# Optimization experiments

Measured on AMD Instinct MI355X. Metric: run time of the kernel, lower is better.

Reference implementation:

```python
import jax, jax.numpy as jnp
import numpy as np

QDIM = 1024; KDIM = 2048; NH = 16; HD = QDIM // NH
H = 64; W = 64; B = 8; S2 = 256
EPS = 1e-6; SCALE = HD ** -0.5


def setup_inputs() -> dict:
    key = jax.random.key(0)
    ks = jax.random.split(key, 8)
    def lin(k, fan_in, shape):
        lim = 1.0 / np.sqrt(fan_in)
        return jax.random.uniform(k, shape, jnp.float32, -lim, lim)
    return {
        "x": jax.random.normal(ks[0], (B, H * W, QDIM), jnp.float32),
        "y": jax.random.normal(ks[1], (B, S2, KDIM), jnp.float32),
        "wq": lin(ks[2], QDIM, (QDIM, QDIM)),
        "bq": lin(ks[3], QDIM, (QDIM,)),
        "wkv": lin(ks[4], KDIM, (2 * QDIM, KDIM)),
        "bkv": lin(ks[5], KDIM, (2 * QDIM,)),
        "wo": lin(ks[6], QDIM, (QDIM, QDIM)),
        "bo": lin(ks[7], QDIM, (QDIM,)),
        "qn_g": jnp.ones((HD,), jnp.float32),
        "qn_b": jnp.zeros((HD,), jnp.float32),
        "kn_g": jnp.ones((HD,), jnp.float32),
        "kn_b": jnp.zeros((HD,), jnp.float32),
    }


def _layernorm(t, g, b):
    mu = t.mean(-1, keepdims=True)
    var = ((t - mu) ** 2).mean(-1, keepdims=True)
    return (t - mu) * jax.lax.rsqrt(var + EPS) * g + b


def _rope_2d_angles():
    # Lumina-style 2D rotary: head_dim//2 complex freqs per position,
    # interleaving H-axis and W-axis frequencies along the pair dim.
    d4 = HD // 4
    inv = 1.0 / (10000.0 ** (np.arange(0, HD // 2, 2, dtype=np.float32) / (HD // 2)))  # (d4,)
    fh = np.outer(np.arange(H, dtype=np.float32), inv)  # (H, d4)
    fw = np.outer(np.arange(W, dtype=np.float32), inv)  # (W, d4)
    ang = np.stack([
        np.broadcast_to(fh[:, None, :], (H, W, d4)),
        np.broadcast_to(fw[None, :, :], (H, W, d4)),
    ], axis=-1).reshape(H, W, HD // 2)  # interleaved h,w,h,w,...
    return jnp.asarray(np.cos(ang)), jnp.asarray(np.sin(ang))


def reference(x, y, wq, bq, wkv, bkv, wo, bo, qn_g, qn_b, kn_g, kn_b):
    b, s1, c = x.shape
    q = (x @ wq.T + bq).reshape(b, s1, NH, HD).transpose(0, 2, 1, 3)          # (b, nh, s1, hd)
    kv = (y @ wkv.T + bkv).reshape(b, -1, 2, NH, HD).transpose(0, 2, 3, 1, 4)  # (b, 2, nh, s2, hd)
    k, v = kv[:, 0], kv[:, 1]
    q = _layernorm(q, qn_g, qn_b)
    k = _layernorm(k, kn_g, kn_b)
    # inline 2D RoPE on Q only (complex mult on interleaved pairs)
    cos, sin = _rope_2d_angles()                                               # (H, W, hd//2)
    qr = q.reshape(b, NH, H, W, HD // 2, 2)
    qe, qo = qr[..., 0], qr[..., 1]
    q = jnp.stack([qe * cos - qo * sin, qe * sin + qo * cos], axis=-1).reshape(b, NH, s1, HD)
    attn = jax.nn.softmax((q * SCALE) @ jnp.swapaxes(k, -2, -1), axis=-1)      # (b, nh, s1, s2)
    out = (attn @ v).transpose(0, 2, 1, 3).reshape(b, s1, c)
    return out @ wo.T + bo
```

## Files before the change

kernel.cpp:

```cpp
#include <hip/hip_runtime.h>
#include <hip/hip_bf16.h>

typedef __bf16 bf16x8 __attribute__((ext_vector_type(8)));
typedef __bf16 bf16x4 __attribute__((ext_vector_type(4)));
typedef float f32x4 __attribute__((ext_vector_type(4)));

__device__ __forceinline__ void async_copy16(__bf16* lds_base, const __bf16* g) {
  __builtin_amdgcn_global_load_lds(
      (const __attribute__((address_space(1))) void*)g,
      (__attribute__((address_space(3))) void*)lds_base, 16, 0, 0);
}

__global__ __launch_bounds__(256) void cvt_bf16(const float* __restrict__ in,
                                                __bf16* __restrict__ out, int n4) {
  int i = blockIdx.x * 256 + threadIdx.x;
  if (i >= n4) return;
  float4 v = ((const float4*)in)[i];
  bf16x4 o;
  o.x = (__bf16)v.x; o.y = (__bf16)v.y; o.z = (__bf16)v.z; o.w = (__bf16)v.w;
  ((bf16x4*)out)[i] = o;
}

template<bool STORE_BF16>
__global__ __launch_bounds__(256) void gemm_bt(const __bf16* __restrict__ A,
                                               const __bf16* __restrict__ Bw,
                                               const float* __restrict__ bias,
                                               void* __restrict__ Cp,
                                               int M, int N, int K) {
  __shared__ __align__(16) __bf16 sA[128 * 64];
  __shared__ __align__(16) __bf16 sB[128 * 64];
  const int tid = threadIdx.x;
  const int lane = tid & 63;
  const int w = tid >> 6;
  const int wr = w >> 1, wc = w & 1;
  const int l15 = lane & 15, q4 = lane >> 4;
  const int bm = blockIdx.x, bn = blockIdx.y;

  f32x4 acc[4][4] = {};

  for (int k0 = 0; k0 < K; k0 += 64) {
    __syncthreads();
#pragma unroll
    for (int it = 0; it < 4; ++it) {
      int chunk = it * 256 + tid;
      int row = chunk >> 3, c8 = chunk & 7;
      int ldsbase = (it * 256 + w * 64) * 8;
      async_copy16(sA + ldsbase, A + (size_t)(bm * 128 + row) * K + k0 + c8 * 8);
      async_copy16(sB + ldsbase, Bw + (size_t)(bn * 128 + row) * K + k0 + c8 * 8);
    }
    __syncthreads();
#pragma unroll
    for (int kk = 0; kk < 2; ++kk) {
      bf16x8 af[4], bfr[4];
#pragma unroll
      for (int i = 0; i < 4; ++i)
        af[i] = *(const bf16x8*)(sA + (wr * 64 + i * 16 + l15) * 64 + kk * 32 + q4 * 8);
#pragma unroll
      for (int j = 0; j < 4; ++j)
        bfr[j] = *(const bf16x8*)(sB + (wc * 64 + j * 16 + l15) * 64 + kk * 32 + q4 * 8);
#pragma unroll
      for (int i = 0; i < 4; ++i)
#pragma unroll
        for (int j = 0; j < 4; ++j)
          acc[i][j] = __builtin_amdgcn_mfma_f32_16x16x32_bf16(af[i], bfr[j], acc[i][j], 0, 0, 0);
    }
  }
#pragma unroll
  for (int j = 0; j < 4; ++j) {
    const int col = bn * 128 + wc * 64 + j * 16 + l15;
    const float bv = bias[col];
#pragma unroll
    for (int i = 0; i < 4; ++i) {
      const int row0 = bm * 128 + wr * 64 + i * 16 + q4 * 4;
#pragma unroll
      for (int r = 0; r < 4; ++r) {
        float v = acc[i][j][r] + bv;
        size_t off = (size_t)(row0 + r) * N + col;
        if (STORE_BF16) ((__bf16*)Cp)[off] = (__bf16)v;
        else            ((float*)Cp)[off]  = v;
      }
    }
  }
}

template<int KK, bool STORE_BF16>
__global__ __launch_bounds__(512, 2) void gemm_bt_big(const __bf16* __restrict__ A,
                                                      const __bf16* __restrict__ Bw,
                                                      const float* __restrict__ bias,
                                                      void* __restrict__ Cp,
                                                      int N) {
  static_assert(KK % 32 == 0 && KK / 32 >= 4, "KK");
  constexpr int NT = KK / 32;
  __shared__ __align__(16) __bf16 sA[4 * 256 * 32];
  __shared__ __align__(16) __bf16 sB[4 * 256 * 32];
  const int tid = threadIdx.x;
  const int lane = tid & 63;
  const int w = tid >> 6;
  const int wr = w >> 2, wc = w & 3;
  const int l15 = lane & 15, q4 = lane >> 4;
  const int bm = blockIdx.x, bn = blockIdx.y;

  const int r0 = tid >> 2;
  const int csw = (tid & 3) ^ (r0 & 3);
  const __bf16* gA0 = A + (size_t)(bm * 256 + r0) * KK + csw * 8;
  const __bf16* gA1 = gA0 + (size_t)128 * KK;
  const __bf16* gB0 = Bw + (size_t)(bn * 256 + r0) * KK + csw * 8;
  const __bf16* gB1 = gB0 + (size_t)128 * KK;
  const int lds_w0 = (w * 64) * 8;
  const int lds_w1 = (512 + w * 64) * 8;

  const int qsw = (q4 ^ (l15 & 3)) * 8;
  const int aBase = (wr * 128 + l15) * 32 + qsw;
  const int bBase = (wc * 64 + l15) * 32 + qsw;

  f32x4 acc[8][4] = {};

#pragma unroll
  for (int t = 0; t < 3; ++t) {
    async_copy16(sA + t * 8192 + lds_w0, gA0 + t * 32);
    async_copy16(sA + t * 8192 + lds_w1, gA1 + t * 32);
    async_copy16(sB + t * 8192 + lds_w0, gB0 + t * 32);
    async_copy16(sB + t * 8192 + lds_w1, gB1 + t * 32);
  }
  asm volatile("s_waitcnt vmcnt(8)" ::: "memory");
  __builtin_amdgcn_s_barrier();
  __builtin_amdgcn_sched_barrier(0);

#pragma unroll 4
  for (int t = 0; t < NT; ++t) {
    const __bf16* sAs = sA + (t & 3) * 8192;
    const __bf16* sBs = sB + (t & 3) * 8192;
    const int ps = (t + 3) & 3;
    const bool pf = (t + 3) < NT;

    bf16x8 af[4], bfrag[4];
#pragma unroll
    for (int m = 0; m < 4; ++m)
      af[m] = *(const bf16x8*)(sAs + aBase + m * 512);
#pragma unroll
    for (int n = 0; n < 4; ++n)
      bfrag[n] = *(const bf16x8*)(sBs + bBase + n * 512);
    if (pf) {
      async_copy16(sA + ps * 8192 + lds_w0, gA0 + (t + 3) * 32);
      async_copy16(sA + ps * 8192 + lds_w1, gA1 + (t + 3) * 32);
    }
    __builtin_amdgcn_s_barrier();
    asm volatile("s_waitcnt lgkmcnt(0)" ::: "memory");
    __builtin_amdgcn_sched_barrier(0);
    __builtin_amdgcn_s_setprio(1);
#pragma unroll
    for (int m = 0; m < 4; ++m)
#pragma unroll
      for (int n = 0; n < 4; ++n)
        acc[m][n] = __builtin_amdgcn_mfma_f32_16x16x32_bf16(af[m], bfrag[n], acc[m][n], 0, 0, 0);
    __builtin_amdgcn_s_setprio(0);
    __builtin_amdgcn_s_barrier();
    __builtin_amdgcn_sched_barrier(0);

    bf16x8 ag[4];
#pragma unroll
    for (int m = 0; m < 4; ++m)
      ag[m] = *(const bf16x8*)(sAs + aBase + 2048 + m * 512);
    if (pf) {
      async_copy16(sB + ps * 8192 + lds_w0, gB0 + (t + 3) * 32);
      async_copy16(sB + ps * 8192 + lds_w1, gB1 + (t + 3) * 32);
    }
    if (pf)                 asm volatile("s_waitcnt vmcnt(8)" ::: "memory");
    else if (t + 3 == NT)   asm volatile("s_waitcnt vmcnt(4)" ::: "memory");
    else if (t + 2 == NT)   asm volatile("s_waitcnt vmcnt(0)" ::: "memory");
    __builtin_amdgcn_s_barrier();
    asm volatile("s_waitcnt lgkmcnt(0)" ::: "memory");
    __builtin_amdgcn_sched_barrier(0);
    __builtin_amdgcn_s_setprio(1);
#pragma unroll
    for (int m = 0; m < 4; ++m)
#pragma unroll
      for (int n = 0; n < 4; ++n)
        acc[4 + m][n] = __builtin_amdgcn_mfma_f32_16x16x32_bf16(ag[m], bfrag[n], acc[4 + m][n], 0, 0, 0);
    __builtin_amdgcn_s_setprio(0);
    __builtin_amdgcn_s_barrier();
    __builtin_amdgcn_sched_barrier(0);
  }

#pragma unroll
  for (int n = 0; n < 4; ++n) {
    const int col = bn * 256 + wc * 64 + n * 16 + l15;
    const float bv = bias[col];
#pragma unroll
    for (int m = 0; m < 8; ++m) {
      const int row0 = bm * 256 + wr * 128 + m * 16 + q4 * 4;
#pragma unroll
      for (int r = 0; r < 4; ++r) {
        float v = acc[m][n][r] + bv;
        size_t off = (size_t)(row0 + r) * N + col;
        if (STORE_BF16) ((__bf16*)Cp)[off] = (__bf16)v;
        else            ((float*)Cp)[off]  = v;
      }
    }
  }
}

__global__ __launch_bounds__(256) void kv_epilogue(const float* __restrict__ kv,
                                                   const float* __restrict__ g,
                                                   const float* __restrict__ bta,
                                                   __bf16* __restrict__ Kd,
                                                   __bf16* __restrict__ VT) {
  const int lane = threadIdx.x & 63;
  const int vec = blockIdx.x * 4 + (threadIdx.x >> 6);
  const int nh = vec & 15;
  const int sv = (vec >> 4) & 1;
  const int row = vec >> 5;
  const int b = row >> 8, s2 = row & 255;
  float v = kv[(size_t)row * 2048 + sv * 1024 + nh * 64 + lane];
  if (sv == 0) {
    float mu = v;
#pragma unroll
    for (int o = 32; o; o >>= 1) mu += __shfl_xor(mu, o);
    mu *= (1.f / 64.f);
    float d = v - mu;
    float va = d * d;
#pragma unroll
    for (int o = 32; o; o >>= 1) va += __shfl_xor(va, o);
    va *= (1.f / 64.f);
    float xn = d * rsqrtf(va + 1e-6f) * g[lane] + bta[lane];
    Kd[(((size_t)b * 16 + nh) * 256 + s2) * 64 + lane] = (__bf16)xn;
  } else {
    VT[(((size_t)b * 16 + nh) * 64 + lane) * 256 + s2] = (__bf16)v;
  }
}

__global__ __launch_bounds__(256) void q_epilogue(const __bf16* __restrict__ qraw,
                                                  const float* __restrict__ g,
                                                  const float* __restrict__ bta,
                                                  __bf16* __restrict__ Q) {
  const int lane = threadIdx.x & 63;
  const int vec = blockIdx.x * 4 + (threadIdx.x >> 6);
  const int nh = vec & 15;
  const int row = vec >> 4;
  float v = (float)qraw[(size_t)row * 1024 + nh * 64 + lane];
  float mu = v;
#pragma unroll
  for (int o = 32; o; o >>= 1) mu += __shfl_xor(mu, o);
  mu *= (1.f / 64.f);
  float d = v - mu;
  float va = d * d;
#pragma unroll
  for (int o = 32; o; o >>= 1) va += __shfl_xor(va, o);
  va *= (1.f / 64.f);
  float xn = d * rsqrtf(va + 1e-6f) * g[lane] + bta[lane];
  const int s1 = row & 4095;
  const int hh = s1 >> 6, wpix = s1 & 63;
  const int t = lane >> 2;
  const int usew = (lane >> 1) & 1;
  float inv = __expf(-(float)t * 0.5756462732485114f);
  float ang = (usew ? (float)wpix : (float)hh) * inv;
  float cc = __cosf(ang), ssn = __sinf(ang);
  float partner = __shfl_xor(xn, 1);
  float rot = xn * cc + partner * ssn * ((lane & 1) ? 1.f : -1.f);
  rot *= 0.125f;
  const int b = row >> 12;
  Q[(((size_t)b * 16 + nh) * 4096 + (size_t)s1) * 64 + lane] = (__bf16)rot;
}

__global__ __launch_bounds__(256) void attn_kernel(const __bf16* __restrict__ Q,
                                                   const __bf16* __restrict__ Kd,
                                                   const __bf16* __restrict__ VT,
                                                   __bf16* __restrict__ O) {
  __shared__ __align__(16) __bf16 sK[256 * 64];
  __shared__ __align__(16) __bf16 sV[64 * 256];
  const int tid = threadIdx.x, lane = tid & 63, w = tid >> 6;
  const int l15 = lane & 15, q4 = lane >> 4;
  const int s7 = l15 & 7;
  const int bh = blockIdx.y;
  const int m0 = blockIdx.x * 64;
  const __bf16* Kg = Kd + (size_t)bh * 256 * 64;
  const __bf16* Vg = VT + (size_t)bh * 64 * 256;
  const __bf16* Qg = Q + ((size_t)bh * 4096 + m0) * 64;
#pragma unroll
  for (int it = 0; it < 8; ++it) {
    int c = it * 256 + tid;
    int kr = c >> 3, kh = c & 7;
    *(uint4*)(sK + kr * 64 + ((kh ^ (kr & 7)) * 8)) = *(const uint4*)(Kg + c * 8);
    int vr = c >> 5, vh = c & 31;
    *(uint4*)(sV + vr * 256 + ((vh ^ (vr & 7)) * 8)) = *(const uint4*)(Vg + c * 8);
  }
  bf16x8 qf0 = *(const bf16x8*)(Qg + (w * 16 + l15) * 64 + q4 * 8);
  bf16x8 qf1 = *(const bf16x8*)(Qg + (w * 16 + l15) * 64 + 32 + q4 * 8);
  __syncthreads();
  f32x4 sacc[16] = {};
#pragma unroll
  for (int mt = 0; mt < 16; ++mt) {
    bf16x8 a0 = *(const bf16x8*)(sK + (mt * 16 + l15) * 64 + ((q4 ^ s7) * 8));
    bf16x8 a1 = *(const bf16x8*)(sK + (mt * 16 + l15) * 64 + (((4 + q4) ^ s7) * 8));
    sacc[mt] = __builtin_amdgcn_mfma_f32_16x16x32_bf16(a0, qf0, sacc[mt], 0, 0, 0);
    sacc[mt] = __builtin_amdgcn_mfma_f32_16x16x32_bf16(a1, qf1, sacc[mt], 0, 0, 0);
  }
  __syncthreads();
  float mx = -1e30f;
#pragma unroll
  for (int mt = 0; mt < 16; ++mt)
#pragma unroll
    for (int r = 0; r < 4; ++r) mx = fmaxf(mx, sacc[mt][r]);
  mx = fmaxf(mx, __shfl_xor(mx, 16));
  mx = fmaxf(mx, __shfl_xor(mx, 32));
  float l = 0.f;
#pragma unroll
  for (int mt = 0; mt < 16; ++mt)
#pragma unroll
    for (int r = 0; r < 4; ++r) {
      float p = __expf(sacc[mt][r] - mx);
      sacc[mt][r] = p;
      l += p;
    }
  l += __shfl_xor(l, 16);
  l += __shfl_xor(l, 32);
  const float linv = 1.f / l;
#pragma unroll
  for (int mt = 0; mt < 16; ++mt) {
    bf16x4 pk;
    pk.x = (__bf16)(sacc[mt][0] * linv);
    pk.y = (__bf16)(sacc[mt][1] * linv);
    pk.z = (__bf16)(sacc[mt][2] * linv);
    pk.w = (__bf16)(sacc[mt][3] * linv);
    int chunk = mt * 2 + (q4 >> 1);
    *(bf16x4*)(sK + (w * 16 + l15) * 256 + ((chunk ^ s7) * 8) + (q4 & 1) * 4) = pk;
  }
  f32x4 oacc[4] = {};
#pragma unroll
  for (int ks = 0; ks < 8; ++ks) {
    int phys = ((ks * 4 + q4) ^ s7) * 8;
    bf16x8 a = *(const bf16x8*)(sK + (w * 16 + l15) * 256 + phys);
#pragma unroll
    for (int j = 0; j < 4; ++j) {
      bf16x8 b = *(const bf16x8*)(sV + (j * 16 + l15) * 256 + phys);
      oacc[j] = __builtin_amdgcn_mfma_f32_16x16x32_bf16(a, b, oacc[j], 0, 0, 0);
    }
  }
  const int b = bh >> 4, nh = bh & 15;
#pragma unroll
  for (int j = 0; j < 4; ++j)
#pragma unroll
    for (int r = 0; r < 4; ++r) {
      size_t off = ((size_t)b * 4096 + m0 + w * 16 + q4 * 4 + r) * 1024
                 + nh * 64 + j * 16 + l15;
      O[off] = (__bf16)oacc[j][r];
    }
}

extern "C" void kernel_launch(void* const* d_in, const int* in_sizes, int n_in,
                              void* d_out, int out_size, void* d_ws, size_t ws_size,
                              hipStream_t stream) {
  const float* x    = (const float*)d_in[0];
  const float* y    = (const float*)d_in[1];
  const float* wq   = (const float*)d_in[2];
  const float* bq   = (const float*)d_in[3];
  const float* wkv  = (const float*)d_in[4];
  const float* bkv  = (const float*)d_in[5];
  const float* wo   = (const float*)d_in[6];
  const float* bo   = (const float*)d_in[7];
  const float* qng  = (const float*)d_in[8];
  const float* qnb  = (const float*)d_in[9];
  const float* kng  = (const float*)d_in[10];
  const float* knb  = (const float*)d_in[11];
  float* out = (float*)d_out;

  char* ws = (char*)d_ws;
  size_t off = 0;
  auto take = [&](size_t bytes) { char* p = ws + off; off += (bytes + 255) & ~(size_t)255; return p; };
  __bf16* xb   = (__bf16*)take((size_t)32768 * 1024 * 2);
  char*  reg1  = take((size_t)32768 * 1024 * 2);
  __bf16* Qb   = (__bf16*)take((size_t)32768 * 1024 * 2);
  __bf16* yb   = (__bf16*)take((size_t)2048 * 2048 * 2);
  __bf16* wqb  = (__bf16*)take((size_t)1024 * 1024 * 2);
  __bf16* wkvb = (__bf16*)take((size_t)2048 * 2048 * 2);
  __bf16* wob  = (__bf16*)take((size_t)1024 * 1024 * 2);
  __bf16* Kb   = (__bf16*)take((size_t)128 * 256 * 64 * 2);
  __bf16* VTb  = (__bf16*)take((size_t)128 * 64 * 256 * 2);
  float*  kvf  = (float*)reg1;
  __bf16* qraw = (__bf16*)reg1;
  __bf16* aout = xb;

  cvt_bf16<<<32768, 256, 0, stream>>>(x,   xb,   8388608);
  cvt_bf16<<<4096,  256, 0, stream>>>(y,   yb,   1048576);
  cvt_bf16<<<1024,  256, 0, stream>>>(wq,  wqb,  262144);
  cvt_bf16<<<4096,  256, 0, stream>>>(wkv, wkvb, 1048576);
  cvt_bf16<<<1024,  256, 0, stream>>>(wo,  wob,  262144);

  gemm_bt<false><<<dim3(16, 16), 256, 0, stream>>>(yb, wkvb, bkv, kvf, 2048, 2048, 2048);
  kv_epilogue<<<16384, 256, 0, stream>>>(kvf, kng, knb, Kb, VTb);

  gemm_bt_big<1024, true><<<dim3(128, 4), 512, 0, stream>>>(xb, wqb, bq, qraw, 1024);
  q_epilogue<<<131072, 256, 0, stream>>>(qraw, qng, qnb, Qb);

  attn_kernel<<<dim3(64, 128), 256, 0, stream>>>(Qb, Kb, VTb, aout);

  gemm_bt_big<1024, false><<<dim3(128, 4), 512, 0, stream>>>(aout, wob, bo, out, 1024);
}
```

Measured before the change: 681.6 us.

## Fuse Q layernorm and RoPE into GEMM epilogue; restructure big GEMM pipeline

```diff
diff --git a/kernel.cpp b/kernel.cpp
--- a/kernel.cpp
+++ b/kernel.cpp
@@ -83,16 +83,18 @@
   }
 }
 
-template<int KK, bool STORE_BF16>
-__global__ __launch_bounds__(512, 2) void gemm_bt_big(const __bf16* __restrict__ A,
-                                                      const __bf16* __restrict__ Bw,
-                                                      const float* __restrict__ bias,
-                                                      void* __restrict__ Cp,
-                                                      int N) {
-  static_assert(KK % 32 == 0 && KK / 32 >= 4, "KK");
-  constexpr int NT = KK / 32;
-  __shared__ __align__(16) __bf16 sA[4 * 256 * 32];
-  __shared__ __align__(16) __bf16 sB[4 * 256 * 32];
+template<int KK, int EPI>
+__global__ __launch_bounds__(512, 2) void gemm_big(const __bf16* __restrict__ A,
+                                                   const __bf16* __restrict__ Bw,
+                                                   const float* __restrict__ bias,
+                                                   void* __restrict__ Cp,
+                                                   const float* __restrict__ g,
+                                                   const float* __restrict__ bt,
+                                                   int N) {
+  constexpr int NT = KK / 64;
+  static_assert(NT >= 3, "need >=3 K-tiles");
+  __shared__ __align__(16) __bf16 sA[2][256 * 64];
+  __shared__ __align__(16) __bf16 sB[2][256 * 64];
   const int tid = threadIdx.x;
   const int lane = tid & 63;
   const int w = tid >> 6;
@@ -100,50 +102,76 @@
   const int l15 = lane & 15, q4 = lane >> 4;
   const int bm = blockIdx.x, bn = blockIdx.y;
 
-  const int r0 = tid >> 2;
-  const int csw = (tid & 3) ^ (r0 & 3);
-  const __bf16* gA0 = A + (size_t)(bm * 256 + r0) * KK + csw * 8;
-  const __bf16* gA1 = gA0 + (size_t)128 * KK;
-  const __bf16* gB0 = Bw + (size_t)(bn * 256 + r0) * KK + csw * 8;
-  const __bf16* gB1 = gB0 + (size_t)128 * KK;
-  const int lds_w0 = (w * 64) * 8;
-  const int lds_w1 = (512 + w * 64) * 8;
-
-  const int qsw = (q4 ^ (l15 & 3)) * 8;
-  const int aBase = (wr * 128 + l15) * 32 + qsw;
-  const int bBase = (wc * 64 + l15) * 32 + qsw;
+  const int rl = lane >> 3;
+  const int cs = (lane & 7) ^ rl;
+  const __bf16* Ag = A + (size_t)(bm * 256) * KK + cs * 8;
+  const __bf16* Bg = Bw + (size_t)(bn * 256) * KK + cs * 8;
+  const int gbA = w * 8;
+  const int gbB = (w & 3) * 8 + (w >> 2) * 64;
+
+  auto STAGE_A = [&](int bb, int t, int h) {
+    int gb = gbA + h * 64;
+    async_copy16(&sA[bb][gb * 64],         Ag + (size_t)(gb + rl) * KK + t * 64);
+    async_copy16(&sA[bb][(gb + 128) * 64], Ag + (size_t)(gb + 128 + rl) * KK + t * 64);
+  };
+  auto STAGE_B = [&](int bb, int t, int h) {
+    int gb = gbB + h * 32;
+    async_copy16(&sB[bb][gb * 64],         Bg + (size_t)(gb + rl) * KK + t * 64);
+    async_copy16(&sB[bb][(gb + 128) * 64], Bg + (size_t)(gb + 128 + rl) * KK + t * 64);
+  };
+
+  const int pc0 = ((q4) ^ (l15 & 7)) * 8;
+  const int pc1 = ((4 + q4) ^ (l15 & 7)) * 8;
+  const int arow0 = (wr * 128 + l15) * 64;
+  const int brow0 = (wc * 64 + l15) * 64;
 
   f32x4 acc[8][4] = {};
 
-#pragma unroll
-  for (int t = 0; t < 3; ++t) {
-    async_copy16(sA + t * 8192 + lds_w0, gA0 + t * 32);
-    async_copy16(sA + t * 8192 + lds_w1, gA1 + t * 32);
-    async_copy16(sB + t * 8192 + lds_w0, gB0 + t * 32);
-    async_copy16(sB + t * 8192 + lds_w1, gB1 + t * 32);
-  }
-  asm volatile("s_waitcnt vmcnt(8)" ::: "memory");
+  STAGE_A(0, 0, 0); STAGE_B(0, 0, 0); STAGE_B(0, 0, 1); STAGE_A(0, 0, 1);
+  STAGE_A(1, 1, 0); STAGE_B(1, 1, 0);
+  asm volatile("s_waitcnt vmcnt(4)" ::: "memory");
   __builtin_amdgcn_s_barrier();
   __builtin_amdgcn_sched_barrier(0);
 
-#pragma unroll 4
+#pragma unroll 2
   for (int t = 0; t < NT; ++t) {
-    const __bf16* sAs = sA + (t & 3) * 8192;
-    const __bf16* sBs = sB + (t & 3) * 8192;
-    const int ps = (t + 3) & 3;
-    const bool pf = (t + 3) < NT;
-
-    bf16x8 af[4], bfrag[4];
+    const int cb = t & 1, nb = cb ^ 1;
+    const __bf16* sAc = sA[cb];
+    const __bf16* sBc = sB[cb];
+    bf16x8 a[4][2], b0[2][2], b1[2][2];
+
+#pragma unroll
+    for (int m = 0; m < 4; ++m) {
+      a[m][0] = *(const bf16x8*)(sAc + arow0 + m * 1024 + pc0);
+      a[m][1] = *(const bf16x8*)(sAc + arow0 + m * 1024 + pc1);
+    }
+#pragma unroll
+    for (int n = 0; n < 2; ++n) {
+      b0[n][0] = *(const bf16x8*)(sBc + brow0 + n * 1024 + pc0);
+      b0[n][1] = *(const bf16x8*)(sBc + brow0 + n * 1024 + pc1);
+    }
+    if (t + 1 < NT) STAGE_B(nb, t + 1, 1);
+    __builtin_amdgcn_s_barrier();
+    asm volatile("s_waitcnt lgkmcnt(0)" ::: "memory");
+    __builtin_amdgcn_sched_barrier(0);
+    __builtin_amdgcn_s_setprio(1);
 #pragma unroll
     for (int m = 0; m < 4; ++m)
-      af[m] = *(const bf16x8*)(sAs + aBase + m * 512);
-#pragma unroll
-    for (int n = 0; n < 4; ++n)
-      bfrag[n] = *(const bf16x8*)(sBs + bBase + n * 512);
-    if (pf) {
-      async_copy16(sA + ps * 8192 + lds_w0, gA0 + (t + 3) * 32);
-      async_copy16(sA + ps * 8192 + lds_w1, gA1 + (t + 3) * 32);
-    }
+#pragma unroll
+      for (int n = 0; n < 2; ++n) {
+        acc[m][n] = __builtin_amdgcn_mfma_f32_16x16x32_bf16(a[m][0], b0[n][0], acc[m][n], 0, 0, 0);
+        acc[m][n] = __builtin_amdgcn_mfma_f32_16x16x32_bf16(a[m][1], b0[n][1], acc[m][n], 0, 0, 0);
+      }
+    __builtin_amdgcn_s_setprio(0);
+    __builtin_amdgcn_s_barrier();
+    __builtin_amdgcn_sched_barrier(0);
+
+#pragma unroll
+    for (int n = 0; n < 2; ++n) {
+      b1[n][0] = *(const bf16x8*)(sBc + brow0 + (2 + n) * 1024 + pc0);
+      b1[n][1] = *(const bf16x8*)(sBc + brow0 + (2 + n) * 1024 + pc1);
+    }
+    if (t + 1 < NT) STAGE_A(nb, t + 1, 1);
     __builtin_amdgcn_s_barrier();
     asm volatile("s_waitcnt lgkmcnt(0)" ::: "memory");
     __builtin_amdgcn_sched_barrier(0);
@@ -151,50 +179,108 @@
 #pragma unroll
     for (int m = 0; m < 4; ++m)
 #pragma unroll
-      for (int n = 0; n < 4; ++n)
-        acc[m][n] = __builtin_amdgcn_mfma_f32_16x16x32_bf16(af[m], bfrag[n], acc[m][n], 0, 0, 0);
+      for (int n = 0; n < 2; ++n) {
+        acc[m][2 + n] = __builtin_amdgcn_mfma_f32_16x16x32_bf16(a[m][0], b1[n][0], acc[m][2 + n], 0, 0, 0);
+        acc[m][2 + n] = __builtin_amdgcn_mfma_f32_16x16x32_bf16(a[m][1], b1[n][1], acc[m][2 + n], 0, 0, 0);
+      }
     __builtin_amdgcn_s_setprio(0);
     __builtin_amdgcn_s_barrier();
     __builtin_amdgcn_sched_barrier(0);
 
-    bf16x8 ag[4];
+#pragma unroll
+    for (int m = 0; m < 4; ++m) {
+      a[m][0] = *(const bf16x8*)(sAc + arow0 + (4 + m) * 1024 + pc0);
+      a[m][1] = *(const bf16x8*)(sAc + arow0 + (4 + m) * 1024 + pc1);
+    }
+    if (t + 2 < NT) STAGE_A(cb, t + 2, 0);
+    __builtin_amdgcn_s_barrier();
+    asm volatile("s_waitcnt lgkmcnt(0)" ::: "memory");
+    __builtin_amdgcn_sched_barrier(0);
+    __builtin_amdgcn_s_setprio(1);
 #pragma unroll
     for (int m = 0; m < 4; ++m)
-      ag[m] = *(const bf16x8*)(sAs + aBase + 2048 + m * 512);
-    if (pf) {
-      async_copy16(sB + ps * 8192 + lds_w0, gB0 + (t + 3) * 32);
-      async_copy16(sB + ps * 8192 + lds_w1, gB1 + (t + 3) * 32);
-    }
-    if (pf)                 asm volatile("s_waitcnt vmcnt(8)" ::: "memory");
-    else if (t + 3 == NT)   asm volatile("s_waitcnt vmcnt(4)" ::: "memory");
-    else if (t + 2 == NT)   asm volatile("s_waitcnt vmcnt(0)" ::: "memory");
-    __builtin_amdgcn_s_barrier();
-    asm volatile("s_waitcnt lgkmcnt(0)" ::: "memory");
+#pragma unroll
+      for (int n = 0; n < 2; ++n) {
+        acc[4 + m][n] = __builtin_amdgcn_mfma_f32_16x16x32_bf16(a[m][0], b0[n][0], acc[4 + m][n], 0, 0, 0);
+        acc[4 + m][n] = __builtin_amdgcn_mfma_f32_16x16x32_bf16(a[m][1], b0[n][1], acc[4 + m][n], 0, 0, 0);
+      }
+    __builtin_amdgcn_s_setprio(0);
+    __builtin_amdgcn_s_barrier();
+    __builtin_amdgcn_sched_barrier(0);
+
+    if (t + 2 < NT) STAGE_B(cb, t + 2, 0);
+    if (t + 2 < NT)      { asm volatile("s_waitcnt vmcnt(4)" ::: "memory"); }
+    else if (t + 1 < NT) { asm volatile("s_waitcnt vmcnt(0)" ::: "memory"); }
+    __builtin_amdgcn_s_barrier();
     __builtin_amdgcn_sched_barrier(0);
     __builtin_amdgcn_s_setprio(1);
 #pragma unroll
     for (int m = 0; m < 4; ++m)
 #pragma unroll
-      for (int n = 0; n < 4; ++n)
-        acc[4 + m][n] = __builtin_amdgcn_mfma_f32_16x16x32_bf16(ag[m], bfrag[n], acc[4 + m][n], 0, 0, 0);
+      for (int n = 0; n < 2; ++n) {
+        acc[4 + m][2 + n] = __builtin_amdgcn_mfma_f32_16x16x32_bf16(a[m][0], b1[n][0], acc[4 + m][2 + n], 0, 0, 0);
+        acc[4 + m][2 + n] = __builtin_amdgcn_mfma_f32_16x16x32_bf16(a[m][1], b1[n][1], acc[4 + m][2 + n], 0, 0, 0);
+      }
     __builtin_amdgcn_s_setprio(0);
     __builtin_amdgcn_s_barrier();
     __builtin_amdgcn_sched_barrier(0);
   }
 
-#pragma unroll
-  for (int n = 0; n < 4; ++n) {
-    const int col = bn * 256 + wc * 64 + n * 16 + l15;
-    const float bv = bias[col];
+  if (EPI == 0) {
+#pragma unroll
+    for (int n = 0; n < 4; ++n) {
+      const int col = bn * 256 + wc * 64 + n * 16 + l15;
+      const float bv = bias[col];
+#pragma unroll
+      for (int m = 0; m < 8; ++m) {
+        const int row0 = bm * 256 + wr * 128 + m * 16 + q4 * 4;
+#pragma unroll
+        for (int r = 0; r < 4; ++r)
+          ((float*)Cp)[(size_t)(row0 + r) * N + col] = acc[m][n][r] + bv;
+      }
+    }
+  } else {
+    const int nh = bn * 4 + wc;
+    const int usew = (l15 >> 1) & 1;
+    const float sgn = (l15 & 1) ? 1.f : -1.f;
+    float gq[4], bqv[4], inv[4], bv[4];
+#pragma unroll
+    for (int n = 0; n < 4; ++n) {
+      const int d = n * 16 + l15;
+      gq[n] = g[d]; bqv[n] = bt[d];
+      bv[n] = bias[nh * 64 + d];
+      inv[n] = __expf(-(float)(d >> 2) * 0.5756462732485114f);
+    }
 #pragma unroll
     for (int m = 0; m < 8; ++m) {
-      const int row0 = bm * 256 + wr * 128 + m * 16 + q4 * 4;
 #pragma unroll
       for (int r = 0; r < 4; ++r) {
-        float v = acc[m][n][r] + bv;
-        size_t off = (size_t)(row0 + r) * N + col;
-        if (STORE_BF16) ((__bf16*)Cp)[off] = (__bf16)v;
-        else            ((float*)Cp)[off]  = v;
+        const int row = bm * 256 + wr * 128 + m * 16 + q4 * 4 + r;
+        const int s1 = row & 4095, bidx = row >> 12;
+        const float base = usew ? (float)(s1 & 63) : (float)(s1 >> 6);
+        float v[4];
+        float sum = 0.f;
+#pragma unroll
+        for (int n = 0; n < 4; ++n) { v[n] = acc[m][n][r] + bv[n]; sum += v[n]; }
+        sum += __shfl_xor(sum, 1); sum += __shfl_xor(sum, 2);
+        sum += __shfl_xor(sum, 4); sum += __shfl_xor(sum, 8);
+        const float mu = sum * (1.f / 64.f);
+        float sq = 0.f;
+#pragma unroll
+        for (int n = 0; n < 4; ++n) { v[n] -= mu; sq += v[n] * v[n]; }
+        sq += __shfl_xor(sq, 1); sq += __shfl_xor(sq, 2);
+        sq += __shfl_xor(sq, 4); sq += __shfl_xor(sq, 8);
+        const float rs = rsqrtf(sq * (1.f / 64.f) + 1e-6f);
+        __bf16* Qrow = (__bf16*)Cp + ((size_t)(bidx * 16 + nh) * 4096 + s1) * 64;
+#pragma unroll
+        for (int n = 0; n < 4; ++n) {
+          const float xn = v[n] * rs * gq[n] + bqv[n];
+          const float ang = base * inv[n];
+          const float cc = __cosf(ang), ssn = __sinf(ang);
+          const float partner = __shfl_xor(xn, 1);
+          const float rot = (xn * cc + partner * ssn * sgn) * 0.125f;
+          Qrow[n * 16 + l15] = (__bf16)rot;
+        }
       }
     }
   }
@@ -227,39 +313,6 @@
   } else {
     VT[(((size_t)b * 16 + nh) * 64 + lane) * 256 + s2] = (__bf16)v;
   }
-}
-
-__global__ __launch_bounds__(256) void q_epilogue(const __bf16* __restrict__ qraw,
-                                                  const float* __restrict__ g,
-                                                  const float* __restrict__ bta,
-                                                  __bf16* __restrict__ Q) {
-  const int lane = threadIdx.x & 63;
-  const int vec = blockIdx.x * 4 + (threadIdx.x >> 6);
-  const int nh = vec & 15;
-  const int row = vec >> 4;
-  float v = (float)qraw[(size_t)row * 1024 + nh * 64 + lane];
-  float mu = v;
-#pragma unroll
-  for (int o = 32; o; o >>= 1) mu += __shfl_xor(mu, o);
-  mu *= (1.f / 64.f);
-  float d = v - mu;
-  float va = d * d;
-#pragma unroll
-  for (int o = 32; o; o >>= 1) va += __shfl_xor(va, o);
-  va *= (1.f / 64.f);
-  float xn = d * rsqrtf(va + 1e-6f) * g[lane] + bta[lane];
-  const int s1 = row & 4095;
-  const int hh = s1 >> 6, wpix = s1 & 63;
-  const int t = lane >> 2;
-  const int usew = (lane >> 1) & 1;
-  float inv = __expf(-(float)t * 0.5756462732485114f);
-  float ang = (usew ? (float)wpix : (float)hh) * inv;
-  float cc = __cosf(ang), ssn = __sinf(ang);
-  float partner = __shfl_xor(xn, 1);
-  float rot = xn * cc + partner * ssn * ((lane & 1) ? 1.f : -1.f);
-  rot *= 0.125f;
-  const int b = row >> 12;
-  Q[(((size_t)b * 16 + nh) * 4096 + (size_t)s1) * 64 + lane] = (__bf16)rot;
 }
 
 __global__ __launch_bounds__(256) void attn_kernel(const __bf16* __restrict__ Q,
@@ -377,7 +430,6 @@
   __bf16* Kb   = (__bf16*)take((size_t)128 * 256 * 64 * 2);
   __bf16* VTb  = (__bf16*)take((size_t)128 * 64 * 256 * 2);
   float*  kvf  = (float*)reg1;
-  __bf16* qraw = (__bf16*)reg1;
   __bf16* aout = xb;
 
   cvt_bf16<<<32768, 256, 0, stream>>>(x,   xb,   8388608);
@@ -389,10 +441,9 @@
   gemm_bt<false><<<dim3(16, 16), 256, 0, stream>>>(yb, wkvb, bkv, kvf, 2048, 2048, 2048);
   kv_epilogue<<<16384, 256, 0, stream>>>(kvf, kng, knb, Kb, VTb);
 
-  gemm_bt_big<1024, true><<<dim3(128, 4), 512, 0, stream>>>(xb, wqb, bq, qraw, 1024);
-  q_epilogue<<<131072, 256, 0, stream>>>(qraw, qng, qnb, Qb);
+  gemm_big<1024, 2><<<dim3(128, 4), 512, 0, stream>>>(xb, wqb, bq, Qb, qng, qnb, 1024);
 
   attn_kernel<<<dim3(64, 128), 256, 0, stream>>>(Qb, Kb, VTb, aout);
 
-  gemm_bt_big<1024, false><<<dim3(128, 4), 512, 0, stream>>>(aout, wob, bo, out, 1024);
-}
+  gemm_big<1024, 0><<<dim3(128, 4), 512, 0, stream>>>(aout, wob, bo, out, nullptr, nullptr, 1024);
+}
```

New measurement: 600.0 us. -12.0%, faster.

## Pipeline KV projection GEMM with 4-stage async LDS ring and swizzle

Applied to the files above, without the earlier changes.

```diff
diff --git a/kernel.cpp b/kernel.cpp
--- a/kernel.cpp
+++ b/kernel.cpp
@@ -21,50 +21,71 @@
   ((bf16x4*)out)[i] = o;
 }
 
-template<bool STORE_BF16>
-__global__ __launch_bounds__(256) void gemm_bt(const __bf16* __restrict__ A,
-                                               const __bf16* __restrict__ Bw,
-                                               const float* __restrict__ bias,
-                                               void* __restrict__ Cp,
-                                               int M, int N, int K) {
-  __shared__ __align__(16) __bf16 sA[128 * 64];
-  __shared__ __align__(16) __bf16 sB[128 * 64];
-  const int tid = threadIdx.x;
-  const int lane = tid & 63;
-  const int w = tid >> 6;
+__global__ __launch_bounds__(256, 1) void kv_gemm(const __bf16* __restrict__ A,
+                                                  const __bf16* __restrict__ Bw,
+                                                  const float* __restrict__ bias,
+                                                  float* __restrict__ Cp,
+                                                  int M, int N, int K) {
+  __shared__ __align__(16) __bf16 sA[4][128 * 32];
+  __shared__ __align__(16) __bf16 sB[4][128 * 32];
+  const int tid = threadIdx.x, lane = tid & 63, w = tid >> 6;
   const int wr = w >> 1, wc = w & 1;
   const int l15 = lane & 15, q4 = lane >> 4;
   const int bm = blockIdx.x, bn = blockIdx.y;
 
+  const int r0 = tid >> 2, c0 = tid & 3;
+  const int cs = c0 ^ (r0 & 3);
+  const __bf16* Ag = A + (size_t)(bm * 128 + r0) * K + cs * 8;
+  const __bf16* Bg = Bw + (size_t)(bn * 128 + r0) * K + cs * 8;
+  const int ldsb0 = (w * 64) * 8;
+  const int ldsb1 = (256 + w * 64) * 8;
+
+  auto STAGE = [&](int slot, int t) {
+    async_copy16(sA[slot] + ldsb0, Ag + (size_t)t * 32);
+    async_copy16(sA[slot] + ldsb1, Ag + (size_t)64 * K + t * 32);
+    async_copy16(sB[slot] + ldsb0, Bg + (size_t)t * 32);
+    async_copy16(sB[slot] + ldsb1, Bg + (size_t)64 * K + t * 32);
+  };
+
+  const int pc = (q4 ^ (l15 & 3)) * 8;
+  const int arow = (wr * 64 + l15) * 32;
+  const int brow = (wc * 64 + l15) * 32;
+
   f32x4 acc[4][4] = {};
-
-  for (int k0 = 0; k0 < K; k0 += 64) {
-    __syncthreads();
-#pragma unroll
-    for (int it = 0; it < 4; ++it) {
-      int chunk = it * 256 + tid;
-      int row = chunk >> 3, c8 = chunk & 7;
-      int ldsbase = (it * 256 + w * 64) * 8;
-      async_copy16(sA + ldsbase, A + (size_t)(bm * 128 + row) * K + k0 + c8 * 8);
-      async_copy16(sB + ldsbase, Bw + (size_t)(bn * 128 + row) * K + k0 + c8 * 8);
-    }
-    __syncthreads();
-#pragma unroll
-    for (int kk = 0; kk < 2; ++kk) {
-      bf16x8 af[4], bfr[4];
-#pragma unroll
-      for (int i = 0; i < 4; ++i)
-        af[i] = *(const bf16x8*)(sA + (wr * 64 + i * 16 + l15) * 64 + kk * 32 + q4 * 8);
+  const int NT = K / 32;
+
+  STAGE(0, 0); STAGE(1, 1); STAGE(2, 2);
+  asm volatile("s_waitcnt vmcnt(8)" ::: "memory");
+  __builtin_amdgcn_s_barrier();
+  __builtin_amdgcn_sched_barrier(0);
+
+#pragma unroll 4
+  for (int t = 0; t < NT; ++t) {
+    const __bf16* At = sA[t & 3];
+    const __bf16* Bt = sB[t & 3];
+    bf16x8 af[4], bfr[4];
+#pragma unroll
+    for (int i = 0; i < 4; ++i) af[i]  = *(const bf16x8*)(At + arow + i * 512 + pc);
+#pragma unroll
+    for (int j = 0; j < 4; ++j) bfr[j] = *(const bf16x8*)(Bt + brow + j * 512 + pc);
+    if (t + 3 < NT) STAGE((t + 3) & 3, t + 3);
+    if (t + 3 < NT)      { asm volatile("s_waitcnt vmcnt(8)" ::: "memory"); }
+    else if (t + 2 < NT) { asm volatile("s_waitcnt vmcnt(4)" ::: "memory"); }
+    else if (t + 1 < NT) { asm volatile("s_waitcnt vmcnt(0)" ::: "memory"); }
+    __builtin_amdgcn_s_barrier();
+    asm volatile("s_waitcnt lgkmcnt(0)" ::: "memory");
+    __builtin_amdgcn_sched_barrier(0);
+    __builtin_amdgcn_s_setprio(1);
+#pragma unroll
+    for (int i = 0; i < 4; ++i)
 #pragma unroll
       for (int j = 0; j < 4; ++j)
-        bfr[j] = *(const bf16x8*)(sB + (wc * 64 + j * 16 + l15) * 64 + kk * 32 + q4 * 8);
-#pragma unroll
-      for (int i = 0; i < 4; ++i)
-#pragma unroll
-        for (int j = 0; j < 4; ++j)
-          acc[i][j] = __builtin_amdgcn_mfma_f32_16x16x32_bf16(af[i], bfr[j], acc[i][j], 0, 0, 0);
-    }
-  }
+        acc[i][j] = __builtin_amdgcn_mfma_f32_16x16x32_bf16(af[i], bfr[j], acc[i][j], 0, 0, 0);
+    __builtin_amdgcn_s_setprio(0);
+    __builtin_amdgcn_s_barrier();
+    __builtin_amdgcn_sched_barrier(0);
+  }
+
 #pragma unroll
   for (int j = 0; j < 4; ++j) {
     const int col = bn * 128 + wc * 64 + j * 16 + l15;
@@ -73,12 +94,8 @@
     for (int i = 0; i < 4; ++i) {
       const int row0 = bm * 128 + wr * 64 + i * 16 + q4 * 4;
 #pragma unroll
-      for (int r = 0; r < 4; ++r) {
-        float v = acc[i][j][r] + bv;
-        size_t off = (size_t)(row0 + r) * N + col;
-        if (STORE_BF16) ((__bf16*)Cp)[off] = (__bf16)v;
-        else            ((float*)Cp)[off]  = v;
-      }
+      for (int r = 0; r < 4; ++r)
+        Cp[(size_t)(row0 + r) * N + col] = acc[i][j][r] + bv;
     }
   }
 }
@@ -386,7 +403,7 @@
   cvt_bf16<<<4096,  256, 0, stream>>>(wkv, wkvb, 1048576);
   cvt_bf16<<<1024,  256, 0, stream>>>(wo,  wob,  262144);
 
-  gemm_bt<false><<<dim3(16, 16), 256, 0, stream>>>(yb, wkvb, bkv, kvf, 2048, 2048, 2048);
+  kv_gemm<<<dim3(16, 16), 256, 0, stream>>>(yb, wkvb, bkv, kvf, 2048, 2048, 2048);
   kv_epilogue<<<16384, 256, 0, stream>>>(kvf, kng, knb, Kb, VTb);
 
   gemm_bt_big<1024, true><<<dim3(128, 4), 512, 0, stream>>>(xb, wqb, bq, qraw, 1024);
```

After: 653.7 us. 1.04x faster.
